# Kernel tuning notes

Measured on AMD Instinct MI355X. Metric: run time of the kernel, lower is better.

## Reference

```python
import jax, jax.numpy as jnp
import numpy as np

N_NODES = 40000
N_EDGES = 640000
IN_C = 128
HID = 32
HEADS = 4
OUT_C = 8
NUM_GRAPHS = 64
NEG_SLOPE = 0.2


def setup_inputs() -> dict:
    key = jax.random.key(0)
    ks = jax.random.split(key, 16)
    x = jax.random.normal(ks[0], (N_NODES, IN_C), dtype=jnp.float32)
    edge_index = jax.random.randint(ks[1], (2, N_EDGES), 0, N_NODES, dtype=jnp.int64)
    batch = jnp.sort(jax.random.randint(ks[2], (N_NODES,), 0, NUM_GRAPHS, dtype=jnp.int64))
    s = lambda k, shape, fan_in: jax.random.normal(k, shape, jnp.float32) / np.sqrt(fan_in)
    # conv0: in -> hid, 4 heads, concat
    W0 = s(ks[3], (IN_C, HEADS * HID), IN_C)
    a_src0 = s(ks[4], (HEADS, HID), HID)
    a_dst0 = s(ks[5], (HEADS, HID), HID)
    b0 = jnp.zeros((HEADS * HID,), jnp.float32)
    # conv1: hid*H -> hid, 4 heads, concat
    W1 = s(ks[6], (HEADS * HID, HEADS * HID), HEADS * HID)
    a_src1 = s(ks[7], (HEADS, HID), HID)
    a_dst1 = s(ks[8], (HEADS, HID), HID)
    b1 = jnp.zeros((HEADS * HID,), jnp.float32)
    # conv2: hid*H -> hid, 1 head, no concat
    W2 = s(ks[9], (HEADS * HID, HID), HEADS * HID)
    a_src2 = s(ks[10], (1, HID), HID)
    a_dst2 = s(ks[11], (1, HID), HID)
    b2 = jnp.zeros((HID,), jnp.float32)
    lin1_w = s(ks[12], (HID, IN_C), HID)
    lin1_b = jnp.zeros((IN_C,), jnp.float32)
    lin2_w = s(ks[13], (IN_C, OUT_C), IN_C)
    lin2_b = jnp.zeros((OUT_C,), jnp.float32)
    return dict(x=x, edge_index=edge_index, batch=batch,
                W0=W0, a_src0=a_src0, a_dst0=a_dst0, b0=b0,
                W1=W1, a_src1=a_src1, a_dst1=a_dst1, b1=b1,
                W2=W2, a_src2=a_src2, a_dst2=a_dst2, b2=b2,
                lin1_w=lin1_w, lin1_b=lin1_b, lin2_w=lin2_w, lin2_b=lin2_b)


def gat_conv(x, src, dst, W, a_src, a_dst, b, heads, out_c, concat):
    N = x.shape[0]
    h = (x @ W).reshape(N, heads, out_c)          # [N,H,C]
    als = (h * a_src[None]).sum(-1)               # [N,H]
    ald = (h * a_dst[None]).sum(-1)               # [N,H]
    e = jax.nn.leaky_relu(als[src] + ald[dst], NEG_SLOPE)  # [E,H]
    m = jax.ops.segment_max(e, dst, num_segments=N)
    m = jnp.where(jnp.isfinite(m), m, 0.0)
    p = jnp.exp(e - m[dst])                       # [E,H]
    denom = jax.ops.segment_sum(p, dst, num_segments=N)
    alpha = p / jnp.maximum(denom[dst], 1e-16)
    out = jax.ops.segment_sum(h[src] * alpha[:, :, None], dst, num_segments=N)
    out = out.reshape(N, heads * out_c) if concat else out.mean(axis=1)
    return out + b


def reference(x, edge_index, batch,
              W0, a_src0, a_dst0, b0,
              W1, a_src1, a_dst1, b1,
              W2, a_src2, a_dst2, b2,
              lin1_w, lin1_b, lin2_w, lin2_b):
    N = x.shape[0]
    # PyG GATConv adds self-loops by default
    loop = jnp.arange(N, dtype=edge_index.dtype)
    src = jnp.concatenate([edge_index[0], loop])
    dst = jnp.concatenate([edge_index[1], loop])
    # eval mode: dropout is identity
    h = jax.nn.elu(gat_conv(x, src, dst, W0, a_src0, a_dst0, b0, HEADS, HID, True))
    h = jax.nn.elu(gat_conv(h, src, dst, W1, a_src1, a_dst1, b1, HEADS, HID, True))
    h = jax.nn.elu(gat_conv(h, src, dst, W2, a_src2, a_dst2, b2, 1, HID, False))
    # global mean pool over graphs
    sums = jax.ops.segment_sum(h, batch, num_segments=NUM_GRAPHS)
    cnts = jax.ops.segment_sum(jnp.ones((N, 1), h.dtype), batch, num_segments=NUM_GRAPHS)
    g = sums / jnp.maximum(cnts, 1.0)             # [G, HID]
    g = jax.nn.relu(g @ lin1_w + lin1_b)
    return g @ lin2_w + lin2_b                    # [G, OUT_C]
```

## Files before the change

### kernel.cpp

```cpp
#include <hip/hip_runtime.h>

#define N_NODES 40000
#define N_EDGES 640000
#define E_TOT   (N_EDGES + N_NODES)
#define NUM_GRAPHS 64
#define CAP_SHIFT 6

#define CVTX_BLOCKS 5000
#define CVTW_BLOCKS 144
#define GEMM_BLOCKS 625

#define BINS 157
#define BIN_CAP 5120
#define TBLK 4096
#define A2BLKS ((N_EDGES + TBLK - 1) / TBLK)

typedef __attribute__((ext_vector_type(8))) short bf16x8;
typedef __attribute__((ext_vector_type(4))) float f32x4;
typedef __attribute__((ext_vector_type(8))) unsigned short u16x8;

__device__ inline float bf2f(unsigned short u) {
    union { unsigned int i; float f; } v; v.i = ((unsigned int)u) << 16; return v.f;
}
__device__ inline unsigned short f2bf(float f) {
    union { float f; unsigned int i; } v; v.f = f;
    unsigned int r = v.i + 0x7FFF + ((v.i >> 16) & 1);
    return (unsigned short)(r >> 16);
}


__device__ void binA2_body(int ab, const int* __restrict__ esrc,
                           const int* __restrict__ edst,
                           int* __restrict__ bin_gcnt,
                           unsigned int* __restrict__ bins) {
    __shared__ unsigned int ebuf[TBLK];
    __shared__ int bcnt[BINS];
    __shared__ int scn[256];
    __shared__ int lbase[BINS];
    __shared__ int boff[BINS];
    __shared__ int gbase[BINS];
    int tid = threadIdx.x;
    for (int i = tid; i < BINS; i += 256) bcnt[i] = 0;
    __syncthreads();
    int ebase = ab * TBLK;
    int ecount = N_EDGES - ebase; if (ecount > TBLK) ecount = TBLK;
    unsigned int ent[16];
#pragma unroll
    for (int k = 0; k < 16; ++k) {
        int idx = k * 256 + tid;
        ent[k] = 0xFFFFFFFFu;
        if (idx < ecount) {
            int e = ebase + idx;
            int d = edst[e], s = esrc[e];
            ent[k] = ((unsigned int)(d >> 8) << 24) |
                     ((unsigned int)(d & 255) << 16) | (unsigned int)s;
            atomicAdd(&bcnt[d >> 8], 1);
        }
    }
    __syncthreads();
    scn[tid] = (tid < BINS) ? bcnt[tid] : 0;
    __syncthreads();
    for (int off = 1; off < 256; off <<= 1) {
        int u = (tid >= off) ? scn[tid - off] : 0;
        __syncthreads();
        scn[tid] += u;
        __syncthreads();
    }
    if (tid < BINS) {
        lbase[tid] = scn[tid] - bcnt[tid];
        boff[tid] = 0;
        if (bcnt[tid]) gbase[tid] = atomicAdd(&bin_gcnt[tid], bcnt[tid]);
    }
    __syncthreads();
#pragma unroll
    for (int k = 0; k < 16; ++k) {
        unsigned int e = ent[k];
        if (e != 0xFFFFFFFFu) {
            int bin = e >> 24;
            int pos = lbase[bin] + atomicAdd(&boff[bin], 1);
            ebuf[pos] = e;
        }
    }
    __syncthreads();
    for (int i = tid; i < ecount; i += 256) {
        unsigned int e = ebuf[i];
        int bin = e >> 24;
        bins[bin * BIN_CAP + gbase[bin] + (i - lbase[bin])] = e & 0x00FFFFFFu;
    }
}


__global__ __launch_bounds__(256) void cvt_binA_kernel(const float* __restrict__ x,
                                                       const float* __restrict__ W0,
                                                       const float* __restrict__ W1,
                                                       const float* __restrict__ W2,
                                                       unsigned short* __restrict__ Xb,
                                                       unsigned short* __restrict__ Wt0,
                                                       unsigned short* __restrict__ Wt1,
                                                       unsigned short* __restrict__ Wt2,
                                                       const int* __restrict__ esrc,
                                                       const int* __restrict__ edst,
                                                       int* __restrict__ bin_gcnt,
                                                       unsigned int* __restrict__ bins) {
    int b = blockIdx.x;
    int tid = threadIdx.x;
    if (b < A2BLKS) {
        binA2_body(b, esrc, edst, bin_gcnt, bins);
    } else if (b < A2BLKS + CVTX_BLOCKS) {
        int i = (b - A2BLKS) * 256 + tid;
        float4 v = ((const float4*)x)[i];
        ushort4 o;
        o.x = f2bf(v.x); o.y = f2bf(v.y); o.z = f2bf(v.z); o.w = f2bf(v.w);
        ((ushort4*)Xb)[i] = o;
    } else {
        int idx = (b - A2BLKS - CVTX_BLOCKS) * 256 + tid;
        if (idx < 16384) {
            int n = idx >> 7, k = idx & 127;
            Wt0[idx] = f2bf(W0[k * 128 + n]);
        } else if (idx < 32768) {
            int i = idx - 16384;
            int n = i >> 7, k = i & 127;
            Wt1[i] = f2bf(W1[k * 128 + n]);
        } else if (idx < 36864) {
            int i = idx - 32768;
            int n = i >> 7, k = i & 127;
            Wt2[i] = f2bf(W2[k * 32 + n]);
        }
    }
}


__device__ void binB_body(int bb, const int* __restrict__ bin_gcnt,
                          const unsigned int* __restrict__ bins,
                          int* __restrict__ cnt,
                          unsigned short* __restrict__ psrc) {
    __shared__ unsigned short lbuck[256 * 64];
    __shared__ int lcnt[256];
    int tid = threadIdx.x;
    lcnt[tid] = 0;
    __syncthreads();
    int cntE = bin_gcnt[bb];
    for (int i = tid; i < cntE; i += 256) {
        unsigned int entry = bins[bb * BIN_CAP + i];
        int dl = entry >> 16;
        int pos = atomicAdd(&lcnt[dl], 1);
        lbuck[dl * 64 + pos] = (unsigned short)(entry & 0xFFFFu);
    }
    __syncthreads();
    int node = bb * 256 + tid;
    if (node < N_NODES) {
        int pos = lcnt[tid];
        lbuck[tid * 64 + pos] = (unsigned short)node;
        lcnt[tid] = pos + 1;
    }
    __syncthreads();
    int base = bb * (256 * 64);
    int lim = (bb == BINS - 1) ? ((N_NODES - bb * 256) * 64) : (256 * 64);
    for (int i = tid; i < lim; i += 256)
        psrc[base + i] = lbuck[i];
    if (node < N_NODES) cnt[node] = lcnt[tid];
}


__device__ __forceinline__ void gemm128_body(int blk,
                                             const unsigned short* __restrict__ Xb,
                                             const unsigned short* __restrict__ Wt,
                                             const float* __restrict__ asrc,
                                             const float* __restrict__ adst,
                                             unsigned short* __restrict__ Hb,
                                             float* __restrict__ ALS4,
                                             float* __restrict__ ALD4) {
    int wave = threadIdx.x >> 6;
    int lane = threadIdx.x & 63;
    int l15 = lane & 15;
    int q = lane >> 4;
    int r0 = (blk * 4 + wave) * 16;

    f32x4 acc[8];
#pragma unroll
    for (int t = 0; t < 8; ++t) acc[t] = (f32x4){0.f, 0.f, 0.f, 0.f};

    float asv[8], adv[8];
#pragma unroll
    for (int t = 0; t < 8; ++t) {
        int c = t * 16 + l15;
        asv[t] = asrc[c];
        adv[t] = adst[c];
    }

    const unsigned short* xrow = Xb + (long)(r0 + l15) * 128 + q * 8;
    const unsigned short* wrow = Wt + (long)l15 * 128 + q * 8;
#pragma unroll
    for (int kt = 0; kt < 4; ++kt) {
        bf16x8 a = *(const bf16x8*)(xrow + kt * 32);
#pragma unroll
        for (int t = 0; t < 8; ++t) {
            bf16x8 b = *(const bf16x8*)(wrow + (long)t * 16 * 128 + kt * 32);
            acc[t] = __builtin_amdgcn_mfma_f32_16x16x32_bf16(a, b, acc[t], 0, 0, 0);
        }
    }

#pragma unroll
    for (int t = 0; t < 8; ++t)
#pragma unroll
        for (int i = 0; i < 4; ++i)
            Hb[(long)(r0 + q * 4 + i) * 128 + t * 16 + l15] = f2bf(acc[t][i]);

#pragma unroll
    for (int i = 0; i < 4; ++i) {
        float ps0 = acc[0][i] * asv[0] + acc[1][i] * asv[1];
        float ps1 = acc[2][i] * asv[2] + acc[3][i] * asv[3];
        float ps2 = acc[4][i] * asv[4] + acc[5][i] * asv[5];
        float ps3 = acc[6][i] * asv[6] + acc[7][i] * asv[7];
        float pd0 = acc[0][i] * adv[0] + acc[1][i] * adv[1];
        float pd1 = acc[2][i] * adv[2] + acc[3][i] * adv[3];
        float pd2 = acc[4][i] * adv[4] + acc[5][i] * adv[5];
        float pd3 = acc[6][i] * adv[6] + acc[7][i] * adv[7];
#pragma unroll
        for (int m = 1; m < 16; m <<= 1) {
            ps0 += __shfl_xor(ps0, m, 16); ps1 += __shfl_xor(ps1, m, 16);
            ps2 += __shfl_xor(ps2, m, 16); ps3 += __shfl_xor(ps3, m, 16);
            pd0 += __shfl_xor(pd0, m, 16); pd1 += __shfl_xor(pd1, m, 16);
            pd2 += __shfl_xor(pd2, m, 16); pd3 += __shfl_xor(pd3, m, 16);
        }
        int r = r0 + q * 4 + i;
        if (l15 < 4) {
            float v = (l15 == 0) ? ps0 : (l15 == 1) ? ps1 : (l15 == 2) ? ps2 : ps3;
            ALS4[r * 4 + l15] = v;
        } else if (l15 < 8) {
            int h = l15 - 4;
            float v = (h == 0) ? pd0 : (h == 1) ? pd1 : (h == 2) ? pd2 : pd3;
            ALD4[r * 4 + h] = v;
        }
    }
}

__global__ __launch_bounds__(256) void gemm0_binB_kernel(const unsigned short* __restrict__ Xb,
                                                         const unsigned short* __restrict__ Wt,
                                                         const float* __restrict__ asrc,
                                                         const float* __restrict__ adst,
                                                         unsigned short* __restrict__ Hb,
                                                         float* __restrict__ ALS4,
                                                         float* __restrict__ ALD4,
                                                         const int* __restrict__ bin_gcnt,
                                                         const unsigned int* __restrict__ bins,
                                                         int* __restrict__ cnt,
                                                         unsigned short* __restrict__ psrc) {
    int b = blockIdx.x;
    if (b < BINS) {
        binB_body(b, bin_gcnt, bins, cnt, psrc);
    } else {
        gemm128_body(b - BINS, Xb, Wt, asrc, adst, Hb, ALS4, ALD4);
    }
}

__global__ __launch_bounds__(256) void gemm128_mfma(const unsigned short* __restrict__ Xb,
                                                    const unsigned short* __restrict__ Wt,
                                                    const float* __restrict__ asrc,
                                                    const float* __restrict__ adst,
                                                    unsigned short* __restrict__ Hb,
                                                    float* __restrict__ ALS4,
                                                    float* __restrict__ ALD4) {
    gemm128_body(blockIdx.x, Xb, Wt, asrc, adst, Hb, ALS4, ALD4);
}

__global__ __launch_bounds__(256) void gemm32_mfma(const unsigned short* __restrict__ Xb,
                                                   const unsigned short* __restrict__ Wt2,
                                                   const float* __restrict__ asrc,
                                                   const float* __restrict__ adst,
                                                   unsigned short* __restrict__ H2b,
                                                   float* __restrict__ ALS,
                                                   float* __restrict__ ALD) {
    int wave = threadIdx.x >> 6;
    int lane = threadIdx.x & 63;
    int l15 = lane & 15;
    int q = lane >> 4;
    int r0 = (blockIdx.x * 4 + wave) * 16;

    f32x4 acc[2];
    acc[0] = (f32x4){0.f, 0.f, 0.f, 0.f};
    acc[1] = (f32x4){0.f, 0.f, 0.f, 0.f};

    const unsigned short* xrow = Xb + (long)(r0 + l15) * 128 + q * 8;
    const unsigned short* wrow = Wt2 + (long)l15 * 128 + q * 8;
#pragma unroll
    for (int kt = 0; kt < 4; ++kt) {
        bf16x8 a = *(const bf16x8*)(xrow + kt * 32);
#pragma unroll
        for (int t = 0; t < 2; ++t) {
            bf16x8 b = *(const bf16x8*)(wrow + (long)t * 16 * 128 + kt * 32);
            acc[t] = __builtin_amdgcn_mfma_f32_16x16x32_bf16(a, b, acc[t], 0, 0, 0);
        }
    }

    float as0 = asrc[l15], as1 = asrc[16 + l15];
    float ad0 = adst[l15], ad1 = adst[16 + l15];
#pragma unroll
    for (int t = 0; t < 2; ++t)
#pragma unroll
        for (int i = 0; i < 4; ++i)
            H2b[(long)(r0 + q * 4 + i) * 32 + t * 16 + l15] = f2bf(acc[t][i]);

#pragma unroll
    for (int i = 0; i < 4; ++i) {
        float ps = acc[0][i] * as0 + acc[1][i] * as1;
        float pd = acc[0][i] * ad0 + acc[1][i] * ad1;
#pragma unroll
        for (int m = 1; m < 16; m <<= 1) {
            ps += __shfl_xor(ps, m, 16);
            pd += __shfl_xor(pd, m, 16);
        }
        if (l15 == 0) {
            int r = r0 + q * 4 + i;
            ALS[r] = ps;
            ALD[r] = pd;
        }
    }
}

__global__ __launch_bounds__(256) void agg128(const unsigned short* __restrict__ Hb,
                                              const float* __restrict__ ALS4,
                                              const float* __restrict__ ALD4,
                                              const int* __restrict__ cnt,
                                              const unsigned short* __restrict__ psrc,
                                              const float* __restrict__ bias,
                                              unsigned short* __restrict__ OUTb) {
    int n = blockIdx.x * 4 + (threadIdx.x >> 6);
    n = __builtin_amdgcn_readfirstlane(n);
    if (n >= N_NODES) return;
    int lane = threadIdx.x & 63;
    int sub = lane & 15;
    int q = lane >> 4;
    int hh = sub >> 2;
    float aldh = ALD4[n * 4 + q];
    int j0 = n << CAP_SHIFT;
    int j1 = j0 + __builtin_amdgcn_readfirstlane(cnt[n]);
    f32x4 a0 = (f32x4){0.f, 0.f, 0.f, 0.f};
    f32x4 a1 = (f32x4){0.f, 0.f, 0.f, 0.f};
    float dsum = 0.f;
    int wb = hh * 16 + q;
    for (int jb = j0; jb < j1; jb += 16) {
        int j = jb + sub;
        int jc = (j < j1) ? j : (j1 - 1);
        int s = (int)psrc[jc];
        float e = ALS4[s * 4 + q] + aldh;
        e = (e > 0.f) ? e : 0.2f * e;
        float w = (j < j1) ? __expf(e) : 0.f;
        int st0 = __shfl(s, q, 16);
        int st1 = __shfl(s, 4 + q, 16);
        int st2 = __shfl(s, 8 + q, 16);
        int st3 = __shfl(s, 12 + q, 16);
        u16x8 h0 = *(const u16x8*)(Hb + (long)st0 * 128 + sub * 8);
        u16x8 h1 = *(const u16x8*)(Hb + (long)st1 * 128 + sub * 8);
        u16x8 h2 = *(const u16x8*)(Hb + (long)st2 * 128 + sub * 8);
        u16x8 h3 = *(const u16x8*)(Hb + (long)st3 * 128 + sub * 8);
        float w0 = __shfl(w, wb, 64);
        float w1 = __shfl(w, wb + 4, 64);
        float w2 = __shfl(w, wb + 8, 64);
        float w3 = __shfl(w, wb + 12, 64);
        dsum += (w0 + w1) + (w2 + w3);
#pragma unroll
        for (int k = 0; k < 4; ++k) {
            a0[k] += w0 * bf2f(h0[k]) + w1 * bf2f(h1[k])
                   + w2 * bf2f(h2[k]) + w3 * bf2f(h3[k]);
            a1[k] += w0 * bf2f(h0[k + 4]) + w1 * bf2f(h1[k + 4])
                   + w2 * bf2f(h2[k + 4]) + w3 * bf2f(h3[k + 4]);
        }
    }
#pragma unroll
    for (int m = 16; m <= 32; m <<= 1) {
        dsum += __shfl_xor(dsum, m, 64);
#pragma unroll
        for (int k = 0; k < 4; ++k) {
            a0[k] += __shfl_xor(a0[k], m, 64);
            a1[k] += __shfl_xor(a1[k], m, 64);
        }
    }
    if (q == 0) {
        float inv = 1.0f / dsum;
        u16x8 ob;
#pragma unroll
        for (int k = 0; k < 4; ++k) {
            float o = a0[k] * inv + bias[sub * 8 + k];
            o = (o > 0.f) ? o : (__expf(o) - 1.f);
            ob[k] = f2bf(o);
            float o2 = a1[k] * inv + bias[sub * 8 + 4 + k];
            o2 = (o2 > 0.f) ? o2 : (__expf(o2) - 1.f);
            ob[k + 4] = f2bf(o2);
        }
        *(u16x8*)(OUTb + (long)n * 128 + sub * 8) = ob;
    }
}

__global__ __launch_bounds__(256) void agg32(const unsigned short* __restrict__ H2b,
                                             const float* __restrict__ ALS,
                                             const float* __restrict__ ALD,
                                             const int* __restrict__ cnt,
                                             const unsigned short* __restrict__ psrc,
                                             const float* __restrict__ bias,
                                             float* __restrict__ OUT) {
    int wv = blockIdx.x * 4 + (threadIdx.x >> 6);
    int lane = threadIdx.x & 63;
    int col = lane & 31;
    int half = lane >> 5;
    int e16 = lane & 15;
    int n = wv * 2 + half;
    if (n >= N_NODES) return;
    float aldn = ALD[n];
    int j0 = n << CAP_SHIFT;
    int j1 = j0 + cnt[n];
    float a = 0.f, dsum = 0.f;
    for (int jb = j0; jb < j1; jb += 16) {
        int j = jb + e16;
        int jc = (j < j1) ? j : (j1 - 1);
        int s = (int)psrc[jc];
        float e = ALS[s] + aldn;
        e = (e > 0.f) ? e : 0.2f * e;
        float w = (j < j1) ? __expf(e) : 0.f;
        int st[16]; float wt[16];
#pragma unroll
        for (int t = 0; t < 16; ++t) {
            st[t] = __shfl(s, t, 16);
            wt[t] = __shfl(w, t, 16);
        }
        unsigned short hv[16];
#pragma unroll
        for (int t = 0; t < 16; ++t)
            hv[t] = H2b[st[t] * 32 + col];
#pragma unroll
        for (int t = 0; t < 16; ++t) {
            dsum += wt[t];
            a += wt[t] * bf2f(hv[t]);
        }
    }
    float o = a / dsum + bias[col];
    o = (o > 0.f) ? o : (__expf(o) - 1.f);
    OUT[n * 32 + col] = o;
}

__global__ __launch_bounds__(256) void pool_kernel(const float* __restrict__ H3,
                                                   const int* __restrict__ batch,
                                                   float* __restrict__ gsum,
                                                   float* __restrict__ gcnt) {
    const int CHUNK = 40;
    int gid = (blockIdx.x * 256 + threadIdx.x) >> 5;
    int c = threadIdx.x & 31;
    int n0 = gid * CHUNK;
    if (n0 >= N_NODES) return;
    int n1 = n0 + CHUNK;
    if (n1 > N_NODES) n1 = N_NODES;
    int cur = batch[n0];
    float acc = 0.f;
    int cnt = 0;
    for (int n = n0; n < n1; ++n) {
        int b = batch[n];
        if (b != cur) {
            atomicAdd(&gsum[cur * 32 + c], acc);
            if (c == 0) atomicAdd(&gcnt[cur], (float)cnt);
            cur = b; acc = 0.f; cnt = 0;
        }
        acc += H3[n * 32 + c];
        cnt++;
    }
    atomicAdd(&gsum[cur * 32 + c], acc);
    if (c == 0) atomicAdd(&gcnt[cur], (float)cnt);
}

__global__ __launch_bounds__(256) void mlp_kernel(const float* __restrict__ gsum,
                                                  const float* __restrict__ gcnt,
                                                  const float* __restrict__ l1w,
                                                  const float* __restrict__ l1b,
                                                  const float* __restrict__ l2w,
                                                  const float* __restrict__ l2b,
                                                  float* __restrict__ out) {
    __shared__ float g[NUM_GRAPHS * 32];
    __shared__ float t1[NUM_GRAPHS * 128];
    int tid = threadIdx.x;
    for (int i = tid; i < NUM_GRAPHS * 32; i += 256) {
        float c = gcnt[i >> 5];
        g[i] = gsum[i] / fmaxf(c, 1.0f);
    }
    __syncthreads();
    for (int i = tid; i < NUM_GRAPHS * 128; i += 256) {
        int r = i >> 7, j = i & 127;
        float a = l1b[j];
        for (int k = 0; k < 32; ++k) a += g[r * 32 + k] * l1w[k * 128 + j];
        t1[i] = fmaxf(a, 0.f);
    }
    __syncthreads();
    for (int i = tid; i < NUM_GRAPHS * 8; i += 256) {
        int r = i >> 3, j = i & 7;
        float a = l2b[j];
        for (int k = 0; k < 128; ++k) a += t1[r * 128 + k] * l2w[k * 8 + j];
        out[i] = a;
    }
}


extern "C" void kernel_launch(void* const* d_in, const int* in_sizes, int n_in,
                              void* d_out, int out_size, void* d_ws, size_t ws_size,
                              hipStream_t stream) {
    const float* x      = (const float*)d_in[0];
    const int*   eidx   = (const int*)d_in[1];
    const int*   batch  = (const int*)d_in[2];
    const float* W0     = (const float*)d_in[3];
    const float* asrc0  = (const float*)d_in[4];
    const float* adst0  = (const float*)d_in[5];
    const float* b0     = (const float*)d_in[6];
    const float* W1     = (const float*)d_in[7];
    const float* asrc1  = (const float*)d_in[8];
    const float* adst1  = (const float*)d_in[9];
    const float* b1     = (const float*)d_in[10];
    const float* W2     = (const float*)d_in[11];
    const float* asrc2  = (const float*)d_in[12];
    const float* adst2  = (const float*)d_in[13];
    const float* b2     = (const float*)d_in[14];
    const float* l1w    = (const float*)d_in[15];
    const float* l1b    = (const float*)d_in[16];
    const float* l2w    = (const float*)d_in[17];
    const float* l2b    = (const float*)d_in[18];
    float* out = (float*)d_out;

    const int* esrc = eidx;
    const int* edst = eidx + N_EDGES;

    float* ALS  = (float*)d_ws;
    float* ALD  = ALS + N_NODES * 4;
    float* h3   = ALD + N_NODES * 4;
    int* cnt    = (int*)(h3 + (long)N_NODES * 32);
    int* bin_gcnt = cnt + N_NODES;
    float* gsum = (float*)(bin_gcnt + BINS);
    float* gcnt = gsum + NUM_GRAPHS * 32;
    unsigned int* bins = (unsigned int*)(gcnt + NUM_GRAPHS);
    unsigned short* psrc = (unsigned short*)(bins + (long)BINS * BIN_CAP);
    uintptr_t p = (uintptr_t)(psrc + ((long)N_NODES << CAP_SHIFT));
    p = (p + 15) & ~(uintptr_t)15;
    unsigned short* Xb   = (unsigned short*)p;
    unsigned short* Hb   = Xb + (long)N_NODES * 128;
    unsigned short* OUTb = Hb + (long)N_NODES * 128;
    unsigned short* H2b  = OUTb + (long)N_NODES * 128;
    unsigned short* Wt0  = H2b + (long)N_NODES * 32;
    unsigned short* Wt1  = Wt0 + 128 * 128;
    unsigned short* Wt2  = Wt1 + 128 * 128;

    size_t zbytes = (size_t)(BINS + NUM_GRAPHS * 32 + NUM_GRAPHS) * 4;
    hipMemsetAsync(bin_gcnt, 0, zbytes, stream);

    cvt_binA_kernel<<<A2BLKS + CVTX_BLOCKS + CVTW_BLOCKS, 256, 0, stream>>>(
        x, W0, W1, W2, Xb, Wt0, Wt1, Wt2, esrc, edst, bin_gcnt, bins);

    gemm0_binB_kernel<<<BINS + GEMM_BLOCKS, 256, 0, stream>>>(
        Xb, Wt0, asrc0, adst0, Hb, ALS, ALD, bin_gcnt, bins, cnt, psrc);
    agg128<<<10000, 256, 0, stream>>>(Hb, ALS, ALD, cnt, psrc, b0, OUTb);

    gemm128_mfma<<<GEMM_BLOCKS, 256, 0, stream>>>(OUTb, Wt1, asrc1, adst1, Hb, ALS, ALD);
    agg128<<<10000, 256, 0, stream>>>(Hb, ALS, ALD, cnt, psrc, b1, OUTb);

    gemm32_mfma<<<GEMM_BLOCKS, 256, 0, stream>>>(OUTb, Wt2, asrc2, adst2, H2b, ALS, ALD);
    agg32<<<5000, 256, 0, stream>>>(H2b, ALS, ALD, cnt, psrc, b2, h3);

    pool_kernel<<<125, 256, 0, stream>>>(h3, batch, gsum, gcnt);
    mlp_kernel<<<1, 256, 0, stream>>>(gsum, gcnt, l1w, l1b, l2w, l2b, out);
}
```

Measured before the change: 272.4 us.

## Precompute per-node edge weights once and restructure GAT aggregation loops

In agg128, each wave now loads all of a node's neighbour indices at once (one lane per edge, up to the 64-slot capacity). It computes the four per-head attention weights with a single float4 ALS load and stages them in LDS, so the inner loop no longer recomputes exp and shuffles per 16-edge chunk. In agg32, each wave now handles one node instead of two, with the two half-waves splitting the edges and combining their results by a final xor-shuffle; the grid is doubled to match. The aim is to cut redundant psrc/ALS loads, exp work and shuffle traffic. The cost is more LDS use, per-slot branch divergence, and a reliance on degree never exceeding 64.

```diff
diff --git a/kernel.cpp b/kernel.cpp
--- a/kernel.cpp
+++ b/kernel.cpp
@@ -325,68 +325,73 @@
                                               const unsigned short* __restrict__ psrc,
                                               const float* __restrict__ bias,
                                               unsigned short* __restrict__ OUTb) {
-    int n = blockIdx.x * 4 + (threadIdx.x >> 6);
+    __shared__ float ws[4][4][68];
+    int wv = threadIdx.x >> 6;
+    int n = blockIdx.x * 4 + wv;
     n = __builtin_amdgcn_readfirstlane(n);
     if (n >= N_NODES) return;
     int lane = threadIdx.x & 63;
     int sub = lane & 15;
-    int q = lane >> 4;
+    int q2 = lane >> 4;
     int hh = sub >> 2;
-    float aldh = ALD4[n * 4 + q];
     int j0 = n << CAP_SHIFT;
-    int j1 = j0 + __builtin_amdgcn_readfirstlane(cnt[n]);
+    int deg = __builtin_amdgcn_readfirstlane(cnt[n]);
+    int jc = (lane < deg) ? (j0 + lane) : (j0 + deg - 1);
+    int s_all = (int)psrc[jc];
+    float4 ald = *(const float4*)(ALD4 + (long)n * 4);
+    float w0v = 0.f, w1v = 0.f, w2v = 0.f, w3v = 0.f;
+    if (lane < deg) {
+        float4 als = *(const float4*)(ALS4 + (long)s_all * 4);
+        float e0 = als.x + ald.x; e0 = (e0 > 0.f) ? e0 : 0.2f * e0;
+        float e1 = als.y + ald.y; e1 = (e1 > 0.f) ? e1 : 0.2f * e1;
+        float e2 = als.z + ald.z; e2 = (e2 > 0.f) ? e2 : 0.2f * e2;
+        float e3 = als.w + ald.w; e3 = (e3 > 0.f) ? e3 : 0.2f * e3;
+        w0v = __expf(e0); w1v = __expf(e1); w2v = __expf(e2); w3v = __expf(e3);
+    }
+    ws[wv][0][lane] = w0v;
+    ws[wv][1][lane] = w1v;
+    ws[wv][2][lane] = w2v;
+    ws[wv][3][lane] = w3v;
     f32x4 a0 = (f32x4){0.f, 0.f, 0.f, 0.f};
     f32x4 a1 = (f32x4){0.f, 0.f, 0.f, 0.f};
     float dsum = 0.f;
-    int wb = hh * 16 + q;
-    for (int jb = j0; jb < j1; jb += 16) {
-        int j = jb + sub;
-        int jc = (j < j1) ? j : (j1 - 1);
-        int s = (int)psrc[jc];
-        float e = ALS4[s * 4 + q] + aldh;
-        e = (e > 0.f) ? e : 0.2f * e;
-        float w = (j < j1) ? __expf(e) : 0.f;
-        int st0 = __shfl(s, q, 16);
-        int st1 = __shfl(s, 4 + q, 16);
-        int st2 = __shfl(s, 8 + q, 16);
-        int st3 = __shfl(s, 12 + q, 16);
-        u16x8 h0 = *(const u16x8*)(Hb + (long)st0 * 128 + sub * 8);
-        u16x8 h1 = *(const u16x8*)(Hb + (long)st1 * 128 + sub * 8);
-        u16x8 h2 = *(const u16x8*)(Hb + (long)st2 * 128 + sub * 8);
-        u16x8 h3 = *(const u16x8*)(Hb + (long)st3 * 128 + sub * 8);
-        float w0 = __shfl(w, wb, 64);
-        float w1 = __shfl(w, wb + 4, 64);
-        float w2 = __shfl(w, wb + 8, 64);
-        float w3 = __shfl(w, wb + 12, 64);
-        dsum += (w0 + w1) + (w2 + w3);
-#pragma unroll
-        for (int k = 0; k < 4; ++k) {
-            a0[k] += w0 * bf2f(h0[k]) + w1 * bf2f(h1[k])
-                   + w2 * bf2f(h2[k]) + w3 * bf2f(h3[k]);
-            a1[k] += w0 * bf2f(h0[k + 4]) + w1 * bf2f(h1[k + 4])
-                   + w2 * bf2f(h2[k + 4]) + w3 * bf2f(h3[k + 4]);
+    for (int sb = 0; sb < deg; sb += 32) {
+#pragma unroll
+        for (int k = 0; k < 8; ++k) {
+            int slot = sb + k * 4 + q2;
+            int s = __shfl(s_all, slot, 64);
+            float w = ws[wv][hh][slot];
+            if (slot < deg) {
+                u16x8 h = *(const u16x8*)(Hb + (long)s * 128 + sub * 8);
+                dsum += w;
+#pragma unroll
+                for (int t = 0; t < 4; ++t) {
+                    a0[t] += w * bf2f(h[t]);
+                    a1[t] += w * bf2f(h[t + 4]);
+                }
+            }
         }
     }
 #pragma unroll
     for (int m = 16; m <= 32; m <<= 1) {
         dsum += __shfl_xor(dsum, m, 64);
 #pragma unroll
-        for (int k = 0; k < 4; ++k) {
-            a0[k] += __shfl_xor(a0[k], m, 64);
-            a1[k] += __shfl_xor(a1[k], m, 64);
-        }
-    }
-    if (q == 0) {
+        for (int t = 0; t < 4; ++t) {
+            a0[t] += __shfl_xor(a0[t], m, 64);
+            a1[t] += __shfl_xor(a1[t], m, 64);
+        }
+    }
+    if (q2 == 0) {
         float inv = 1.0f / dsum;
         u16x8 ob;
 #pragma unroll
-        for (int k = 0; k < 4; ++k) {
-            float o = a0[k] * inv + bias[sub * 8 + k];
+        for (int t = 0; t < 4; ++t) {
+            float o = a0[t] * inv + bias[sub * 8 + t];
             o = (o > 0.f) ? o : (__expf(o) - 1.f);
-            ob[k] = f2bf(o);
-            float o2 = a1[k] * inv + bias[sub * 8 + 4 + k];
+            ob[t] = f2bf(o);
+            float o2 = a1[t] * inv + bias[sub * 8 + 4 + t];
             o2 = (o2 > 0.f) ? o2 : (__expf(o2) - 1.f);
-            ob[k + 4] = f2bf(o2);
+            ob[t + 4] = f2bf(o2);
         }
         *(u16x8*)(OUTb + (long)n * 128 + sub * 8) = ob;
     }
@@ -399,43 +404,44 @@
                                              const unsigned short* __restrict__ psrc,
                                              const float* __restrict__ bias,
                                              float* __restrict__ OUT) {
-    int wv = blockIdx.x * 4 + (threadIdx.x >> 6);
+    int n = blockIdx.x * 4 + (threadIdx.x >> 6);
+    n = __builtin_amdgcn_readfirstlane(n);
+    if (n >= N_NODES) return;
     int lane = threadIdx.x & 63;
     int col = lane & 31;
-    int half = lane >> 5;
-    int e16 = lane & 15;
-    int n = wv * 2 + half;
-    if (n >= N_NODES) return;
+    int q2 = lane >> 5;
+    int j0 = n << CAP_SHIFT;
+    int deg = __builtin_amdgcn_readfirstlane(cnt[n]);
+    int jc = (lane < deg) ? (j0 + lane) : (j0 + deg - 1);
+    int s_all = (int)psrc[jc];
     float aldn = ALD[n];
-    int j0 = n << CAP_SHIFT;
-    int j1 = j0 + cnt[n];
+    float w = 0.f;
+    if (lane < deg) {
+        float e = ALS[s_all] + aldn;
+        e = (e > 0.f) ? e : 0.2f * e;
+        w = __expf(e);
+    }
     float a = 0.f, dsum = 0.f;
-    for (int jb = j0; jb < j1; jb += 16) {
-        int j = jb + e16;
-        int jc = (j < j1) ? j : (j1 - 1);
-        int s = (int)psrc[jc];
-        float e = ALS[s] + aldn;
-        e = (e > 0.f) ? e : 0.2f * e;
-        float w = (j < j1) ? __expf(e) : 0.f;
-        int st[16]; float wt[16];
-#pragma unroll
-        for (int t = 0; t < 16; ++t) {
-            st[t] = __shfl(s, t, 16);
-            wt[t] = __shfl(w, t, 16);
-        }
-        unsigned short hv[16];
-#pragma unroll
-        for (int t = 0; t < 16; ++t)
-            hv[t] = H2b[st[t] * 32 + col];
-#pragma unroll
-        for (int t = 0; t < 16; ++t) {
-            dsum += wt[t];
-            a += wt[t] * bf2f(hv[t]);
-        }
-    }
-    float o = a / dsum + bias[col];
-    o = (o > 0.f) ? o : (__expf(o) - 1.f);
-    OUT[n * 32 + col] = o;
+    for (int sb = 0; sb < deg; sb += 32) {
+#pragma unroll
+        for (int k = 0; k < 16; ++k) {
+            int slot = sb + k * 2 + q2;
+            int s = __shfl(s_all, slot, 64);
+            float wk = __shfl(w, slot, 64);
+            if (slot < deg) {
+                float h = bf2f(H2b[(long)s * 32 + col]);
+                dsum += wk;
+                a += wk * h;
+            }
+        }
+    }
+    a += __shfl_xor(a, 32, 64);
+    dsum += __shfl_xor(dsum, 32, 64);
+    if (q2 == 0) {
+        float o = a / dsum + bias[col];
+        o = (o > 0.f) ? o : (__expf(o) - 1.f);
+        OUT[n * 32 + col] = o;
+    }
 }
 
 __global__ __launch_bounds__(256) void pool_kernel(const float* __restrict__ H3,
@@ -557,7 +563,7 @@
     agg128<<<10000, 256, 0, stream>>>(Hb, ALS, ALD, cnt, psrc, b1, OUTb);
 
     gemm32_mfma<<<GEMM_BLOCKS, 256, 0, stream>>>(OUTb, Wt2, asrc2, adst2, H2b, ALS, ALD);
-    agg32<<<5000, 256, 0, stream>>>(H2b, ALS, ALD, cnt, psrc, b2, h3);
+    agg32<<<10000, 256, 0, stream>>>(H2b, ALS, ALD, cnt, psrc, b2, h3);
 
     pool_kernel<<<125, 256, 0, stream>>>(h3, batch, gsum, gcnt);
     mlp_kernel<<<1, 256, 0, stream>>>(gsum, gcnt, l1w, l1b, l2w, l2b, out);
```

New measurement: 283.5 us. +4.1%, slower.
